# Kernel optimization log

Measured on AMD Instinct MI355X. Metric: run time of the kernel, lower is better.

## Reference

```python
import jax, jax.numpy as jnp
import numpy as np

SPIKING_T = 8        # args['spiking_t']
V_TH = 1.0           # spikingjelly IFNode default v_threshold
TAU = 2.0            # NonSpikingLIFNode tau
ALPHA = 4.0          # spikingjelly default Sigmoid surrogate alpha
MIN_LOG_STD, MAX_LOG_STD = -20.0, 2.0
LOG_2PI = float(np.log(2.0 * np.pi))

@jax.custom_vjp
def spike(x):
    # Heaviside forward (spikingjelly surrogate.Sigmoid behavior)
    return (x >= 0.0).astype(x.dtype)

def _spike_fwd(x):
    return spike(x), x

def _spike_bwd(x, g):
    s = jax.nn.sigmoid(ALPHA * x)
    return (g * ALPHA * s * (1.0 - s),)

spike.defvjp(_spike_fwd, _spike_bwd)


def setup_inputs() -> dict:
    key = jax.random.key(0)
    ks = jax.random.split(key, 8)
    B, N, H, A = 8192, 128, 1024, 32
    def lin_w(k, fan_in, fan_out):
        return jax.random.normal(k, (fan_in, fan_out), dtype=jnp.float32) / jnp.sqrt(float(fan_in))
    return {
        "state": jax.random.normal(ks[0], (B, N), dtype=jnp.float32),
        "w1": lin_w(ks[1], N, H),
        "b1": jnp.full((H,), 1e-6, dtype=jnp.float32),
        "w2": lin_w(ks[2], H, H),
        "b2": jnp.full((H,), 1e-6, dtype=jnp.float32),
        "w3": lin_w(ks[3], H, 2 * A),
        "b3": jnp.full((2 * A,), 1e-6, dtype=jnp.float32),
        "eps": jax.random.normal(ks[4], (B, A), dtype=jnp.float32),
    }


def reference(state, w1, b1, w2, b2, w3, b3, eps):
    B = state.shape[0]
    H = w1.shape[1]
    O = w3.shape[1]
    v1 = jnp.zeros((B, H), state.dtype)
    v2 = jnp.zeros((B, H), state.dtype)
    v3 = jnp.zeros((B, O), state.dtype)

    def step(carry, _):
        v1, v2, v3 = carry
        # IF node 1: charge, fire, hard reset to 0
        h1 = v1 + state @ w1 + b1
        s1 = spike(h1 - V_TH)
        v1 = h1 * (1.0 - s1)
        # IF node 2
        h2 = v2 + s1 @ w2 + b2
        s2 = spike(h2 - V_TH)
        v2 = h2 * (1.0 - s2)
        # NonSpiking LIF (decay_input=True, v_reset=0): v += (x - v)/tau
        x3 = s2 @ w3 + b3
        v3 = v3 + (x3 - v3) / TAU
        return (v1, v2, v3), None

    (v1, v2, v3), _ = jax.lax.scan(step, (v1, v2, v3), None, length=SPIKING_T)

    mu, log_std = jnp.split(v3, 2, axis=-1)
    log_std = jnp.clip(log_std, MIN_LOG_STD, MAX_LOG_STD)
    std = jnp.exp(log_std)
    z = mu + std * eps            # Normal rsample
    action = jnp.tanh(z)
    # Normal(mu, std).log_prob(z) = -eps^2/2 - log_std - 0.5*log(2*pi)
    log_prob = (-0.5 * eps * eps - log_std - 0.5 * LOG_2PI) \
               - jnp.log(1.0 - action * action + 1e-7)
    log_prob = jnp.sum(log_prob, axis=-1, keepdims=True)
    return action, log_prob
```

## Files before the change

### kernel.cpp

```cpp
#include <hip/hip_runtime.h>

typedef float    f32x4 __attribute__((ext_vector_type(4)));
typedef int      i32x4 __attribute__((ext_vector_type(4)));
typedef unsigned u32x4 __attribute__((ext_vector_type(4)));

constexpr int Bsz  = 8192;
constexpr int Nin  = 128;
constexpr int Hd   = 1024;
constexpr int Aact = 32;
constexpr int Od   = 64;
constexpr int KC = 384;
constexpr float DELTA = 1.5e-4f;
constexpr unsigned WCAP = 262144;

__global__ void wsplit_all_kernel(const float* __restrict__ w2, const float* __restrict__ w3,
                                  char* __restrict__ p1, char* __restrict__ p2,
                                  char* __restrict__ p3,
                                  char* __restrict__ r1, char* __restrict__ r2,
                                  char* __restrict__ r3,
                                  float* __restrict__ w2tf) {
  const int lane = threadIdx.x;
  const int l15 = lane & 15, quad = lane >> 4;
  const int pn = blockIdx.x;
  const int kb = blockIdx.y;
  const bool isw3 = (pn >= Hd / 16);
  const int pnl = isw3 ? pn - Hd / 16 : pn;
  const float* src = isw3 ? w3 : w2;
  const int N = isw3 ? Od : Hd;
  const int n = pnl * 16 + l15;
  const int k0 = kb * 64 + quad * 16;
  char* d1 = isw3 ? r1 : p1;
  char* d2 = isw3 ? r2 : p2;
  char* d3 = isw3 ? r3 : p3;
  float wv[16];
  char o1[16], o2[16], o3[16];
#pragma unroll
  for (int e = 0; e < 16; ++e) {
    float w = src[(size_t)(k0 + e) * N + n];
    wv[e] = w;
    float m1 = rintf(w * 512.0f);
    float q1 = w - m1 * (1.0f / 512.0f);
    float m2 = rintf(q1 * 65536.0f);
    float q2 = q1 - m2 * (1.0f / 65536.0f);
    float m3 = rintf(q2 * 8388608.0f);
    o1[e] = (char)(int)m1; o2[e] = (char)(int)m2; o3[e] = (char)(int)m3;
  }
  size_t off = ((size_t)pnl * 16 + kb) * 1024 + (size_t)lane * 16;
#pragma unroll
  for (int e = 0; e < 16; ++e) {
    d1[off + e] = o1[e]; d2[off + e] = o2[e]; d3[off + e] = o3[e];
  }
  if (!isw3) {
#pragma unroll
    for (int e = 0; e < 16; ++e)
      w2tf[(size_t)n * Hd + k0 + e] = wv[e];
  }
}

__global__ __launch_bounds__(256)
void x1_kernel(const float* __restrict__ state, const float* __restrict__ w1,
               const float* __restrict__ b1, unsigned char* __restrict__ s1pack) {
  __shared__ float sA[64][129];
  __shared__ float sB[128][68];
  const int m0 = blockIdx.x * 64, n0 = blockIdx.y * 64;
  const int tid = threadIdx.x;
  for (int idx = tid; idx < 64 * 32; idx += 256) {
    int r = idx >> 5, c4 = (idx & 31) << 2;
    float4 v = *(const float4*)(state + (size_t)(m0 + r) * Nin + c4);
    sA[r][c4] = v.x; sA[r][c4 + 1] = v.y; sA[r][c4 + 2] = v.z; sA[r][c4 + 3] = v.w;
  }
  for (int idx = tid; idx < 128 * 16; idx += 256) {
    int r = idx >> 4, c4 = (idx & 15) << 2;
    *(float4*)&sB[r][c4] = *(const float4*)(w1 + (size_t)r * Hd + n0 + c4);
  }
  __syncthreads();
  const int tx = tid & 15, ty = tid >> 4;
  float acc[4][4] = {};
  for (int k = 0; k < 128; ++k) {
    float a[4];
#pragma unroll
    for (int i = 0; i < 4; ++i) a[i] = sA[ty * 4 + i][k];
    float4 b = *(const float4*)&sB[k][tx * 4];
#pragma unroll
    for (int i = 0; i < 4; ++i) {
      acc[i][0] = __fmaf_rn(a[i], b.x, acc[i][0]);
      acc[i][1] = __fmaf_rn(a[i], b.y, acc[i][1]);
      acc[i][2] = __fmaf_rn(a[i], b.z, acc[i][2]);
      acc[i][3] = __fmaf_rn(a[i], b.w, acc[i][3]);
    }
  }
#pragma unroll
  for (int i = 0; i < 4; ++i) {
    int m = m0 + ty * 4 + i;
    unsigned pack = 0;
#pragma unroll
    for (int j = 0; j < 4; ++j) {
      int n = n0 + tx * 4 + j;
      float x = acc[i][j];
      float bb = b1[n];
      float v = 0.0f;
      unsigned bits = 0;
#pragma unroll
      for (int t = 0; t < 8; ++t) {
        float h = __fadd_rn(__fadd_rn(v, x), bb);
        if (h >= 1.0f) { bits |= (1u << t); v = 0.0f; } else { v = h; }
      }
      pack |= bits << (8 * j);
    }
    *(unsigned*)(s1pack + (size_t)m * Hd + n0 + tx * 4) = pack;
  }
}

__global__ __launch_bounds__(256, 3)
void gemm2i8_kernel(const unsigned char* __restrict__ s1pack,
                    const char* __restrict__ q1, const char* __restrict__ q2,
                    const char* __restrict__ q3,
                    const float* __restrict__ b2,
                    unsigned char* __restrict__ s2p,
                    unsigned* __restrict__ wcnt, unsigned* __restrict__ wlist) {
  constexpr int NKB = Hd / 64;
  const int tid = threadIdx.x;
  const int m0 = blockIdx.x * 64;
  const int n0 = blockIdx.y * 16;
  const int wave = tid >> 6, lane = tid & 63, l15 = lane & 15, quad = lane >> 4;
  const unsigned char* asrc = s1pack
      + (size_t)(m0 + wave * 16 + l15) * Hd + (lane >> 4) * 16;
  const size_t boff = (size_t)blockIdx.y * NKB * 1024 + (size_t)lane * 16;
  const char* bp0 = q1 + boff;
  const char* bp1 = q2 + boff;
  const char* bp2 = q3 + boff;
  i32x4 acc[3][8] = {};

  u32x4 a_cur = *(const u32x4*)asrc;
  i32x4 f0c = *(const i32x4*)bp0;
  i32x4 f1c = *(const i32x4*)bp1;
  i32x4 f2c = *(const i32x4*)bp2;
#pragma unroll
  for (int kb = 0; kb < NKB; ++kb) {
    u32x4 a_nxt = a_cur; i32x4 f0n = f0c, f1n = f1c, f2n = f2c;
    if (kb + 1 < NKB) {
      a_nxt = *(const u32x4*)(asrc + (kb + 1) * 64);
      f0n = *(const i32x4*)(bp0 + (size_t)(kb + 1) * 1024);
      f1n = *(const i32x4*)(bp1 + (size_t)(kb + 1) * 1024);
      f2n = *(const i32x4*)(bp2 + (size_t)(kb + 1) * 1024);
    }
#pragma unroll
    for (int t = 0; t < 8; ++t) {
      i32x4 af;
      af[0] = (int)((a_cur[0] >> t) & 0x01010101u);
      af[1] = (int)((a_cur[1] >> t) & 0x01010101u);
      af[2] = (int)((a_cur[2] >> t) & 0x01010101u);
      af[3] = (int)((a_cur[3] >> t) & 0x01010101u);
      acc[0][t] = __builtin_amdgcn_mfma_i32_16x16x64_i8(af, f0c, acc[0][t], 0, 0, 0);
      acc[1][t] = __builtin_amdgcn_mfma_i32_16x16x64_i8(af, f1c, acc[1][t], 0, 0, 0);
      acc[2][t] = __builtin_amdgcn_mfma_i32_16x16x64_i8(af, f2c, acc[2][t], 0, 0, 0);
    }
    a_cur = a_nxt; f0c = f0n; f1c = f1n; f2c = f2n;
  }
  const int n = n0 + l15;
  const float bb = b2[n];
#pragma unroll
  for (int r = 0; r < 4; ++r) {
    int m = m0 + wave * 16 + quad * 4 + r;
    size_t idx = (size_t)m * Hd + n;
    float v = 0.0f;
    unsigned bits = 0;
#pragma unroll
    for (int t = 0; t < 8; ++t) {
      double ge = (double)acc[0][t][r] * 1.953125e-3
                + (double)acc[1][t][r] * 1.52587890625e-5
                + (double)acc[2][t][r] * 1.1920928955078125e-7;
      float G = (float)ge;
      float h = __fadd_rn(__fadd_rn(v, G), bb);
      if (__builtin_expect(__builtin_fabsf(h - 1.0f) < DELTA, 0)) {
        unsigned pos = atomicAdd(wcnt, 1u);
        if (pos < WCAP) wlist[pos] = (unsigned)idx;
      }
      bool sp = (h >= 1.0f);
      if (sp) bits |= (1u << t);
      v = sp ? 0.0f : h;
    }
    s2p[idx] = (unsigned char)bits;
  }
}

__global__ __launch_bounds__(256)
void fixup_kernel(const unsigned* __restrict__ wcnt, const unsigned* __restrict__ wlist,
                  const unsigned char* __restrict__ s1pack, const float* __restrict__ w2tf,
                  const float* __restrict__ b2, unsigned char* __restrict__ s2p) {
  unsigned cnt = *wcnt;
  if (cnt > WCAP) cnt = WCAP;
  const int tid = threadIdx.x;
  const int lane = tid & 63;
  const int sl = lane / 3, blk3 = lane - sl * 3;
  const int wid = blockIdx.x * (blockDim.x >> 6) + (tid >> 6);
  const int nwaves = gridDim.x * (blockDim.x >> 6);
  for (unsigned base = (unsigned)wid * 21u; base < cnt; base += (unsigned)nwaves * 21u) {
    unsigned site = base + (unsigned)sl;
    bool act = (sl < 21) && (site < cnt);
    unsigned idx = act ? wlist[site] : 0u;
    int m = (int)(idx >> 10), n = (int)(idx & 1023u);
    const unsigned char* prow = s1pack + ((size_t)m << 10);
    const float* col = w2tf + ((size_t)n << 10);
    int kb = blk3 * KC;
    int kend = (blk3 == 2) ? Hd : kb + KC;
    float S[8] = {};
    if (act) {
      for (int k = kb; k < kend; k += 8) {
        float4 wa = *(const float4*)(col + k);
        float4 wb = *(const float4*)(col + k + 4);
        unsigned b0 = *(const unsigned*)(prow + k);
        unsigned b1 = *(const unsigned*)(prow + k + 4);
#pragma unroll
        for (int tau = 0; tau < 8; ++tau) {
          S[tau] = __fadd_rn(S[tau], ((b0 >> tau) & 1)        ? wa.x : 0.0f);
          S[tau] = __fadd_rn(S[tau], ((b0 >> (8 + tau)) & 1)  ? wa.y : 0.0f);
          S[tau] = __fadd_rn(S[tau], ((b0 >> (16 + tau)) & 1) ? wa.z : 0.0f);
          S[tau] = __fadd_rn(S[tau], ((b0 >> (24 + tau)) & 1) ? wa.w : 0.0f);
          S[tau] = __fadd_rn(S[tau], ((b1 >> tau) & 1)        ? wb.x : 0.0f);
          S[tau] = __fadd_rn(S[tau], ((b1 >> (8 + tau)) & 1)  ? wb.y : 0.0f);
          S[tau] = __fadd_rn(S[tau], ((b1 >> (16 + tau)) & 1) ? wb.z : 0.0f);
          S[tau] = __fadd_rn(S[tau], ((b1 >> (24 + tau)) & 1) ? wb.w : 0.0f);
        }
      }
    }
    float G[8];
#pragma unroll
    for (int tau = 0; tau < 8; ++tau) {
      float sB = __shfl(S[tau], lane + 1);
      float sC = __shfl(S[tau], lane + 2);
      G[tau] = __fadd_rn(__fadd_rn(S[tau], sB), sC);
    }
    if (act && blk3 == 0) {
      float bb = b2[n];
      float v = 0.0f;
      unsigned bits = 0;
      for (int tau = 0; tau < 8; ++tau) {
        float h = __fadd_rn(__fadd_rn(v, G[tau]), bb);
        bool sp = (h >= 1.0f);
        if (sp) bits |= (1u << tau);
        v = sp ? 0.0f : h;
      }
      s2p[idx] = (unsigned char)bits;
    }
  }
}

__global__ __launch_bounds__(256, 3)
void gemm3i8_kernel(const unsigned char* __restrict__ s2p,
                    const char* __restrict__ q1, const char* __restrict__ q2,
                    const char* __restrict__ q3,
                    const float* __restrict__ b3, float* __restrict__ v3) {
  constexpr int NKB = Hd / 64;
  const int tid = threadIdx.x;
  const int m0 = blockIdx.x * 64;
  const int n0 = blockIdx.y * 16;
  const int wave = tid >> 6, lane = tid & 63, l15 = lane & 15, quad = lane >> 4;
  const unsigned char* asrc = s2p
      + (size_t)(m0 + wave * 16 + l15) * Hd + (lane >> 4) * 16;
  const size_t boff = (size_t)blockIdx.y * NKB * 1024 + (size_t)lane * 16;
  const char* bp0 = q1 + boff;
  const char* bp1 = q2 + boff;
  const char* bp2 = q3 + boff;
  i32x4 acc[3][8] = {};

  u32x4 a_cur = *(const u32x4*)asrc;
  i32x4 f0c = *(const i32x4*)bp0;
  i32x4 f1c = *(const i32x4*)bp1;
  i32x4 f2c = *(const i32x4*)bp2;
#pragma unroll
  for (int kb = 0; kb < NKB; ++kb) {
    u32x4 a_nxt = a_cur; i32x4 f0n = f0c, f1n = f1c, f2n = f2c;
    if (kb + 1 < NKB) {
      a_nxt = *(const u32x4*)(asrc + (kb + 1) * 64);
      f0n = *(const i32x4*)(bp0 + (size_t)(kb + 1) * 1024);
      f1n = *(const i32x4*)(bp1 + (size_t)(kb + 1) * 1024);
      f2n = *(const i32x4*)(bp2 + (size_t)(kb + 1) * 1024);
    }
#pragma unroll
    for (int t = 0; t < 8; ++t) {
      i32x4 af;
      af[0] = (int)((a_cur[0] >> t) & 0x01010101u);
      af[1] = (int)((a_cur[1] >> t) & 0x01010101u);
      af[2] = (int)((a_cur[2] >> t) & 0x01010101u);
      af[3] = (int)((a_cur[3] >> t) & 0x01010101u);
      acc[0][t] = __builtin_amdgcn_mfma_i32_16x16x64_i8(af, f0c, acc[0][t], 0, 0, 0);
      acc[1][t] = __builtin_amdgcn_mfma_i32_16x16x64_i8(af, f1c, acc[1][t], 0, 0, 0);
      acc[2][t] = __builtin_amdgcn_mfma_i32_16x16x64_i8(af, f2c, acc[2][t], 0, 0, 0);
    }
    a_cur = a_nxt; f0c = f0n; f1c = f1n; f2c = f2n;
  }
  const int n = n0 + l15;
  const float bb = b3[n];
#pragma unroll
  for (int r = 0; r < 4; ++r) {
    int m = m0 + wave * 16 + quad * 4 + r;
    float v = 0.0f;
#pragma unroll
    for (int t = 0; t < 8; ++t) {
      double ge = (double)acc[0][t][r] * 1.953125e-3
                + (double)acc[1][t][r] * 1.52587890625e-5
                + (double)acc[2][t][r] * 1.1920928955078125e-7;
      float x3 = __fadd_rn((float)ge, bb);
      float dd = __fsub_rn(x3, v);
      v = __fadd_rn(v, __fmul_rn(dd, 0.5f));
    }
    v3[(size_t)m * Od + n] = v;
  }
}

__global__ void final_kernel(const float* __restrict__ v3, const float* __restrict__ eps,
                             float* __restrict__ action, float* __restrict__ logp) {
  int tid = threadIdx.x;
  int row = blockIdx.x * 8 + (tid >> 5);
  int j = tid & 31;
  float mu = v3[(size_t)row * Od + j];
  float ls = v3[(size_t)row * Od + 32 + j];
  ls = fminf(fmaxf(ls, -20.0f), 2.0f);
  float sd = (float)exp((double)ls);
  float e  = eps[(size_t)row * Aact + j];
  float z  = __fadd_rn(mu, __fmul_rn(sd, e));
  float a;
  if (__builtin_fabsf(z) >= 7.90531111f) a = __builtin_copysignf(1.0f, z);
  else                                   a = (float)tanh((double)z);
  float aa = __fmul_rn(a, a);
  float u  = __fadd_rn(__fsub_rn(1.0f, aa), 1e-7f);
  float lg = (float)log((double)u);
  float l  = __fmul_rn(__fmul_rn(-0.5f, e), e);
  l = __fsub_rn(l, ls);
  l = __fsub_rn(l, 0.9189385332046727f);
  float term = __fsub_rn(l, lg);
  action[(size_t)row * Aact + j] = a;
  double lp = (double)term;
#pragma unroll
  for (int w = 16; w >= 1; w >>= 1) lp += __shfl_xor(lp, w);
  if (j == 0) logp[row] = (float)lp;
}

extern "C" void kernel_launch(void* const* d_in, const int* in_sizes, int n_in,
                              void* d_out, int out_size, void* d_ws, size_t ws_size,
                              hipStream_t stream) {
  const float* state = (const float*)d_in[0];
  const float* w1 = (const float*)d_in[1];
  const float* b1 = (const float*)d_in[2];
  const float* w2 = (const float*)d_in[3];
  const float* b2 = (const float*)d_in[4];
  const float* w3 = (const float*)d_in[5];
  const float* b3 = (const float*)d_in[6];
  const float* eps = (const float*)d_in[7];
  float* out_action = (float*)d_out;
  float* out_logp = out_action + (size_t)Bsz * Aact;

  char* p = (char*)d_ws;
  auto take = [&](size_t bytes) {
    char* r = p;
    p += (bytes + 255) & ~(size_t)255;
    return r;
  };
  float* v3f = (float*)take((size_t)Bsz * Od * 4);
  unsigned char* s1pack = (unsigned char*)take((size_t)Bsz * Hd);
  unsigned char* s2p = (unsigned char*)take((size_t)Bsz * Hd);
  char* w2q1 = (char*)take((size_t)Hd * Hd);
  char* w2q2 = (char*)take((size_t)Hd * Hd);
  char* w2q3 = (char*)take((size_t)Hd * Hd);
  char* w3q1 = (char*)take((size_t)Hd * Od);
  char* w3q2 = (char*)take((size_t)Hd * Od);
  char* w3q3 = (char*)take((size_t)Hd * Od);
  float* w2tf = (float*)take((size_t)Hd * Hd * 4);
  unsigned* wcnt = (unsigned*)take(8 * 4);
  unsigned* wlist = (unsigned*)take((size_t)WCAP * 4);

  wsplit_all_kernel<<<dim3(Hd / 16 + Od / 16, Hd / 64), 64, 0, stream>>>(
      w2, w3, w2q1, w2q2, w2q3, w3q1, w3q2, w3q3, w2tf);
  x1_kernel<<<dim3(Bsz / 64, Hd / 64), 256, 0, stream>>>(state, w1, b1, s1pack);
  hipMemsetAsync(wcnt, 0, 8 * 4, stream);

  gemm2i8_kernel<<<dim3(Bsz / 64, Hd / 16), 256, 0, stream>>>(s1pack, w2q1, w2q2, w2q3,
                                                              b2, s2p, wcnt, wlist);
  fixup_kernel<<<128, 256, 0, stream>>>(wcnt, wlist, s1pack, w2tf, b2, s2p);

  gemm3i8_kernel<<<dim3(Bsz / 64, Od / 16), 256, 0, stream>>>(s2p, w3q1, w3q2, w3q3,
                                                              b3, v3f);
  final_kernel<<<Bsz / 8, 256, 0, stream>>>(v3f, eps, out_action, out_logp);
}
```

Measured before the change: 325.9 us.

## Stage GEMM2 operands through LDS with async loads and fuse auxiliary kernels

The layer-2 int8 GEMM now stages activation and weight tiles into shared memory with direct global-to-LDS loads in a three-deep ring buffer. Each of three waves loads one weight plane that the four waves then share, which removes the duplicated per-wave weight fetches. The weight-splitting kernel is merged with the layer-1 kernel into one prep launch, and that launch also replaces the memset. The layer-3 GEMM is fused with the final tanh/log-prob epilogue, dropping the v3 round trip and two launches. The cost is a barrier on every k-step and hand-written vmcnt waits that depend on exact load counts.

```diff
diff --git a/kernel.cpp b/kernel.cpp
--- a/kernel.cpp
+++ b/kernel.cpp
@@ -3,6 +3,13 @@
 typedef float    f32x4 __attribute__((ext_vector_type(4)));
 typedef int      i32x4 __attribute__((ext_vector_type(4)));
 typedef unsigned u32x4 __attribute__((ext_vector_type(4)));
+
+typedef const __attribute__((address_space(1))) void* gptr_t;
+typedef __attribute__((address_space(3))) void* lptr_t;
+
+__device__ __forceinline__ void gload_lds16(const void* g, void* l) {
+  __builtin_amdgcn_global_load_lds((gptr_t)g, (lptr_t)l, 16, 0, 0);
+}
 
 constexpr int Bsz  = 8192;
 constexpr int Nin  = 128;
@@ -13,57 +20,61 @@
 constexpr float DELTA = 1.5e-4f;
 constexpr unsigned WCAP = 262144;
 
-__global__ void wsplit_all_kernel(const float* __restrict__ w2, const float* __restrict__ w3,
-                                  char* __restrict__ p1, char* __restrict__ p2,
-                                  char* __restrict__ p3,
-                                  char* __restrict__ r1, char* __restrict__ r2,
-                                  char* __restrict__ r3,
-                                  float* __restrict__ w2tf) {
-  const int lane = threadIdx.x;
-  const int l15 = lane & 15, quad = lane >> 4;
-  const int pn = blockIdx.x;
-  const int kb = blockIdx.y;
-  const bool isw3 = (pn >= Hd / 16);
-  const int pnl = isw3 ? pn - Hd / 16 : pn;
-  const float* src = isw3 ? w3 : w2;
-  const int N = isw3 ? Od : Hd;
-  const int n = pnl * 16 + l15;
-  const int k0 = kb * 64 + quad * 16;
-  char* d1 = isw3 ? r1 : p1;
-  char* d2 = isw3 ? r2 : p2;
-  char* d3 = isw3 ? r3 : p3;
-  float wv[16];
-  char o1[16], o2[16], o3[16];
-#pragma unroll
-  for (int e = 0; e < 16; ++e) {
-    float w = src[(size_t)(k0 + e) * N + n];
-    wv[e] = w;
-    float m1 = rintf(w * 512.0f);
-    float q1 = w - m1 * (1.0f / 512.0f);
-    float m2 = rintf(q1 * 65536.0f);
-    float q2 = q1 - m2 * (1.0f / 65536.0f);
-    float m3 = rintf(q2 * 8388608.0f);
-    o1[e] = (char)(int)m1; o2[e] = (char)(int)m2; o3[e] = (char)(int)m3;
-  }
-  size_t off = ((size_t)pnl * 16 + kb) * 1024 + (size_t)lane * 16;
-#pragma unroll
-  for (int e = 0; e < 16; ++e) {
-    d1[off + e] = o1[e]; d2[off + e] = o2[e]; d3[off + e] = o3[e];
-  }
-  if (!isw3) {
-#pragma unroll
-    for (int e = 0; e < 16; ++e)
-      w2tf[(size_t)n * Hd + k0 + e] = wv[e];
-  }
-}
-
 __global__ __launch_bounds__(256)
-void x1_kernel(const float* __restrict__ state, const float* __restrict__ w1,
-               const float* __restrict__ b1, unsigned char* __restrict__ s1pack) {
+void prep_kernel(const float* __restrict__ state, const float* __restrict__ w1,
+                 const float* __restrict__ b1,
+                 const float* __restrict__ w2, const float* __restrict__ w3,
+                 unsigned char* __restrict__ s1pack,
+                 char* __restrict__ p1, char* __restrict__ p2, char* __restrict__ p3,
+                 char* __restrict__ r1, char* __restrict__ r2, char* __restrict__ r3,
+                 float* __restrict__ w2tf, unsigned* __restrict__ wcnt) {
   __shared__ float sA[64][129];
   __shared__ float sB[128][68];
-  const int m0 = blockIdx.x * 64, n0 = blockIdx.y * 64;
   const int tid = threadIdx.x;
+
+  if (blockIdx.x >= 2048) {
+    if (blockIdx.x == 2048 && tid < 8) wcnt[tid] = 0;
+    const int u = (blockIdx.x - 2048) * 4 + (tid >> 6);
+    const int lane = tid & 63;
+    const int l15 = lane & 15, quad = lane >> 4;
+    const int pn = u >> 4;
+    const int kb = u & 15;
+    const bool isw3 = (pn >= Hd / 16);
+    const int pnl = isw3 ? pn - Hd / 16 : pn;
+    const float* src = isw3 ? w3 : w2;
+    const int N = isw3 ? Od : Hd;
+    const int n = pnl * 16 + l15;
+    const int k0 = kb * 64 + quad * 16;
+    char* d1 = isw3 ? r1 : p1;
+    char* d2 = isw3 ? r2 : p2;
+    char* d3 = isw3 ? r3 : p3;
+    float wv[16];
+    char o1[16], o2[16], o3[16];
+#pragma unroll
+    for (int e = 0; e < 16; ++e) {
+      float w = src[(size_t)(k0 + e) * N + n];
+      wv[e] = w;
+      float m1 = rintf(w * 512.0f);
+      float q1 = w - m1 * (1.0f / 512.0f);
+      float m2 = rintf(q1 * 65536.0f);
+      float q2 = q1 - m2 * (1.0f / 65536.0f);
+      float m3 = rintf(q2 * 8388608.0f);
+      o1[e] = (char)(int)m1; o2[e] = (char)(int)m2; o3[e] = (char)(int)m3;
+    }
+    size_t off = ((size_t)pnl * 16 + kb) * 1024 + (size_t)lane * 16;
+#pragma unroll
+    for (int e = 0; e < 16; ++e) {
+      d1[off + e] = o1[e]; d2[off + e] = o2[e]; d3[off + e] = o3[e];
+    }
+    if (!isw3) {
+#pragma unroll
+      for (int e = 0; e < 16; ++e)
+        w2tf[(size_t)n * Hd + k0 + e] = wv[e];
+    }
+    return;
+  }
+
+  const int m0 = (blockIdx.x & 127) * 64, n0 = (blockIdx.x >> 7) * 64;
   for (int idx = tid; idx < 64 * 32; idx += 256) {
     int r = idx >> 5, c4 = (idx & 31) << 2;
     float4 v = *(const float4*)(state + (size_t)(m0 + r) * Nin + c4);
@@ -119,43 +130,52 @@
                     unsigned char* __restrict__ s2p,
                     unsigned* __restrict__ wcnt, unsigned* __restrict__ wlist) {
   constexpr int NKB = Hd / 64;
+  __shared__ __align__(16) unsigned char lA[3][64 * 64];
+  __shared__ __align__(16) char lB[3][3072];
   const int tid = threadIdx.x;
   const int m0 = blockIdx.x * 64;
   const int n0 = blockIdx.y * 16;
   const int wave = tid >> 6, lane = tid & 63, l15 = lane & 15, quad = lane >> 4;
+  const char* bplane = (wave == 0) ? q1 : (wave == 1) ? q2 : q3;
   const unsigned char* asrc = s1pack
-      + (size_t)(m0 + wave * 16 + l15) * Hd + (lane >> 4) * 16;
-  const size_t boff = (size_t)blockIdx.y * NKB * 1024 + (size_t)lane * 16;
-  const char* bp0 = q1 + boff;
-  const char* bp1 = q2 + boff;
-  const char* bp2 = q3 + boff;
+      + (size_t)(m0 + ((tid >> 6) << 4) + (tid & 15)) * Hd + ((tid >> 4) & 3) * 16;
+  const char* bsrc2 = bplane + (size_t)blockIdx.y * NKB * 1024 + (size_t)lane * 16;
   i32x4 acc[3][8] = {};
 
-  u32x4 a_cur = *(const u32x4*)asrc;
-  i32x4 f0c = *(const i32x4*)bp0;
-  i32x4 f1c = *(const i32x4*)bp1;
-  i32x4 f2c = *(const i32x4*)bp2;
+  auto stage = [&](int kb, int buf) {
+    gload_lds16(asrc + kb * 64, &lA[buf][tid * 16]);
+    if (wave < 3)
+      gload_lds16(bsrc2 + (size_t)kb * 1024, &lB[buf][wave * 1024 + lane * 16]);
+  };
+  stage(0, 0); stage(1, 1);
+
 #pragma unroll
   for (int kb = 0; kb < NKB; ++kb) {
-    u32x4 a_nxt = a_cur; i32x4 f0n = f0c, f1n = f1c, f2n = f2c;
-    if (kb + 1 < NKB) {
-      a_nxt = *(const u32x4*)(asrc + (kb + 1) * 64);
-      f0n = *(const i32x4*)(bp0 + (size_t)(kb + 1) * 1024);
-      f1n = *(const i32x4*)(bp1 + (size_t)(kb + 1) * 1024);
-      f2n = *(const i32x4*)(bp2 + (size_t)(kb + 1) * 1024);
-    }
+    const int cur = kb % 3;
+    if (kb < NKB - 1) {
+      if (wave < 3) asm volatile("s_waitcnt vmcnt(2)" ::: "memory");
+      else          asm volatile("s_waitcnt vmcnt(1)" ::: "memory");
+    } else {
+      asm volatile("s_waitcnt vmcnt(0)" ::: "memory");
+    }
+    __builtin_amdgcn_s_barrier();
+    asm volatile("" ::: "memory");
+    u32x4 ad = *(const u32x4*)&lA[cur][wave * 1024 + lane * 16];
+    i32x4 fb0 = *(const i32x4*)&lB[cur][lane * 16];
+    i32x4 fb1 = *(const i32x4*)&lB[cur][1024 + lane * 16];
+    i32x4 fb2 = *(const i32x4*)&lB[cur][2048 + lane * 16];
+    if (kb + 2 < NKB) stage(kb + 2, (kb + 2) % 3);
 #pragma unroll
     for (int t = 0; t < 8; ++t) {
       i32x4 af;
-      af[0] = (int)((a_cur[0] >> t) & 0x01010101u);
-      af[1] = (int)((a_cur[1] >> t) & 0x01010101u);
-      af[2] = (int)((a_cur[2] >> t) & 0x01010101u);
-      af[3] = (int)((a_cur[3] >> t) & 0x01010101u);
-      acc[0][t] = __builtin_amdgcn_mfma_i32_16x16x64_i8(af, f0c, acc[0][t], 0, 0, 0);
-      acc[1][t] = __builtin_amdgcn_mfma_i32_16x16x64_i8(af, f1c, acc[1][t], 0, 0, 0);
-      acc[2][t] = __builtin_amdgcn_mfma_i32_16x16x64_i8(af, f2c, acc[2][t], 0, 0, 0);
-    }
-    a_cur = a_nxt; f0c = f0n; f1c = f1n; f2c = f2n;
+      af[0] = (int)((ad[0] >> t) & 0x01010101u);
+      af[1] = (int)((ad[1] >> t) & 0x01010101u);
+      af[2] = (int)((ad[2] >> t) & 0x01010101u);
+      af[3] = (int)((ad[3] >> t) & 0x01010101u);
+      acc[0][t] = __builtin_amdgcn_mfma_i32_16x16x64_i8(af, fb0, acc[0][t], 0, 0, 0);
+      acc[1][t] = __builtin_amdgcn_mfma_i32_16x16x64_i8(af, fb1, acc[1][t], 0, 0, 0);
+      acc[2][t] = __builtin_amdgcn_mfma_i32_16x16x64_i8(af, fb2, acc[2][t], 0, 0, 0);
+    }
   }
   const int n = n0 + l15;
   const float bb = b2[n];
@@ -247,18 +267,18 @@
 }
 
 __global__ __launch_bounds__(256, 3)
-void gemm3i8_kernel(const unsigned char* __restrict__ s2p,
-                    const char* __restrict__ q1, const char* __restrict__ q2,
-                    const char* __restrict__ q3,
-                    const float* __restrict__ b3, float* __restrict__ v3) {
+void gemm3f_kernel(const unsigned char* __restrict__ s2p,
+                   const char* __restrict__ q1, const char* __restrict__ q2,
+                   const char* __restrict__ q3,
+                   const float* __restrict__ b3, const float* __restrict__ eps,
+                   float* __restrict__ action, float* __restrict__ logp) {
   constexpr int NKB = Hd / 64;
+  __shared__ float sv[16][65];
   const int tid = threadIdx.x;
-  const int m0 = blockIdx.x * 64;
-  const int n0 = blockIdx.y * 16;
+  const int m0 = blockIdx.x * 16;
   const int wave = tid >> 6, lane = tid & 63, l15 = lane & 15, quad = lane >> 4;
-  const unsigned char* asrc = s2p
-      + (size_t)(m0 + wave * 16 + l15) * Hd + (lane >> 4) * 16;
-  const size_t boff = (size_t)blockIdx.y * NKB * 1024 + (size_t)lane * 16;
+  const unsigned char* asrc = s2p + (size_t)(m0 + l15) * Hd + (lane >> 4) * 16;
+  const size_t boff = (size_t)wave * NKB * 1024 + (size_t)lane * 16;
   const char* bp0 = q1 + boff;
   const char* bp1 = q2 + boff;
   const char* bp2 = q3 + boff;
@@ -290,11 +310,11 @@
     }
     a_cur = a_nxt; f0c = f0n; f1c = f1n; f2c = f2n;
   }
-  const int n = n0 + l15;
+  const int n = wave * 16 + l15;
   const float bb = b3[n];
 #pragma unroll
   for (int r = 0; r < 4; ++r) {
-    int m = m0 + wave * 16 + quad * 4 + r;
+    int row = quad * 4 + r;
     float v = 0.0f;
 #pragma unroll
     for (int t = 0; t < 8; ++t) {
@@ -305,36 +325,35 @@
       float dd = __fsub_rn(x3, v);
       v = __fadd_rn(v, __fmul_rn(dd, 0.5f));
     }
-    v3[(size_t)m * Od + n] = v;
-  }
-}
-
-__global__ void final_kernel(const float* __restrict__ v3, const float* __restrict__ eps,
-                             float* __restrict__ action, float* __restrict__ logp) {
-  int tid = threadIdx.x;
-  int row = blockIdx.x * 8 + (tid >> 5);
-  int j = tid & 31;
-  float mu = v3[(size_t)row * Od + j];
-  float ls = v3[(size_t)row * Od + 32 + j];
-  ls = fminf(fmaxf(ls, -20.0f), 2.0f);
-  float sd = (float)exp((double)ls);
-  float e  = eps[(size_t)row * Aact + j];
-  float z  = __fadd_rn(mu, __fmul_rn(sd, e));
-  float a;
-  if (__builtin_fabsf(z) >= 7.90531111f) a = __builtin_copysignf(1.0f, z);
-  else                                   a = (float)tanh((double)z);
-  float aa = __fmul_rn(a, a);
-  float u  = __fadd_rn(__fsub_rn(1.0f, aa), 1e-7f);
-  float lg = (float)log((double)u);
-  float l  = __fmul_rn(__fmul_rn(-0.5f, e), e);
-  l = __fsub_rn(l, ls);
-  l = __fsub_rn(l, 0.9189385332046727f);
-  float term = __fsub_rn(l, lg);
-  action[(size_t)row * Aact + j] = a;
-  double lp = (double)term;
-#pragma unroll
-  for (int w = 16; w >= 1; w >>= 1) lp += __shfl_xor(lp, w);
-  if (j == 0) logp[row] = (float)lp;
+    sv[row][n] = v;
+  }
+  __syncthreads();
+#pragma unroll
+  for (int pass = 0; pass < 2; ++pass) {
+    int row = (pass << 3) + (tid >> 5);
+    int j = tid & 31;
+    float mu = sv[row][j];
+    float ls = sv[row][32 + j];
+    ls = fminf(fmaxf(ls, -20.0f), 2.0f);
+    float sd = (float)exp((double)ls);
+    float e  = eps[(size_t)(m0 + row) * Aact + j];
+    float z  = __fadd_rn(mu, __fmul_rn(sd, e));
+    float a;
+    if (__builtin_fabsf(z) >= 7.90531111f) a = __builtin_copysignf(1.0f, z);
+    else                                   a = (float)tanh((double)z);
+    float aa = __fmul_rn(a, a);
+    float u  = __fadd_rn(__fsub_rn(1.0f, aa), 1e-7f);
+    float lg = (float)log((double)u);
+    float l  = __fmul_rn(__fmul_rn(-0.5f, e), e);
+    l = __fsub_rn(l, ls);
+    l = __fsub_rn(l, 0.9189385332046727f);
+    float term = __fsub_rn(l, lg);
+    action[(size_t)(m0 + row) * Aact + j] = a;
+    double lp = (double)term;
+#pragma unroll
+    for (int w = 16; w >= 1; w >>= 1) lp += __shfl_xor(lp, w);
+    if (j == 0) logp[m0 + row] = (float)lp;
+  }
 }
 
 extern "C" void kernel_launch(void* const* d_in, const int* in_sizes, int n_in,
@@ -357,7 +376,6 @@
     p += (bytes + 255) & ~(size_t)255;
     return r;
   };
-  float* v3f = (float*)take((size_t)Bsz * Od * 4);
   unsigned char* s1pack = (unsigned char*)take((size_t)Bsz * Hd);
   unsigned char* s2p = (unsigned char*)take((size_t)Bsz * Hd);
   char* w2q1 = (char*)take((size_t)Hd * Hd);
@@ -370,16 +388,13 @@
   unsigned* wcnt = (unsigned*)take(8 * 4);
   unsigned* wlist = (unsigned*)take((size_t)WCAP * 4);
 
-  wsplit_all_kernel<<<dim3(Hd / 16 + Od / 16, Hd / 64), 64, 0, stream>>>(
-      w2, w3, w2q1, w2q2, w2q3, w3q1, w3q2, w3q3, w2tf);
-  x1_kernel<<<dim3(Bsz / 64, Hd / 64), 256, 0, stream>>>(state, w1, b1, s1pack);
-  hipMemsetAsync(wcnt, 0, 8 * 4, stream);
-
+  prep_kernel<<<2048 + 272, 256, 0, stream>>>(state, w1, b1, w2, w3, s1pack,
+                                              w2q1, w2q2, w2q3, w3q1, w3q2, w3q3,
+                                              w2tf, wcnt);
   gemm2i8_kernel<<<dim3(Bsz / 64, Hd / 16), 256, 0, stream>>>(s1pack, w2q1, w2q2, w2q3,
                                                               b2, s2p, wcnt, wlist);
   fixup_kernel<<<128, 256, 0, stream>>>(wcnt, wlist, s1pack, w2tf, b2, s2p);
 
-  gemm3i8_kernel<<<dim3(Bsz / 64, Od / 16), 256, 0, stream>>>(s2p, w3q1, w3q2, w3q3,
-                                                              b3, v3f);
-  final_kernel<<<Bsz / 8, 256, 0, stream>>>(v3f, eps, out_action, out_logp);
-}
+  gemm3f_kernel<<<Bsz / 16, 256, 0, stream>>>(s2p, w3q1, w3q2, w3q3, b3, eps,
+                                              out_action, out_logp);
+}
```

Measured after the change: 319.3 us. -2.0%, faster.
